# Optimization experiments

Measured on AMD Instinct MI355X. Metric: run time of the kernel, lower is better.

The kernel has to match this reference:

```python
import jax, jax.numpy as jnp
import numpy as np

DEGREE = 5
A = 1.0
B = 1.0
IN_F = 1024
OUT_F = 1024
BATCH = 8192


def setup_inputs() -> dict:
    key = jax.random.key(0)
    k1, k2, k3, k4 = jax.random.split(key, 4)
    x = jax.random.normal(k1, (BATCH, IN_F), dtype=jnp.float32)
    # base_weight ~ kaiming-uniform-ish scale
    bound_w = 1.0 / np.sqrt(IN_F)
    base_weight = jax.random.uniform(k2, (OUT_F, IN_F), dtype=jnp.float32,
                                     minval=-bound_w, maxval=bound_w)
    std = 1.0 / (IN_F * np.sqrt(DEGREE + 1))
    jacobi_coeffs = std * jax.random.normal(k3, (OUT_F, IN_F, DEGREE + 1), dtype=jnp.float32)
    bias = jax.random.uniform(k4, (OUT_F,), dtype=jnp.float32, minval=-bound_w, maxval=bound_w)
    return {"x": x, "base_weight": base_weight, "jacobi_coeffs": jacobi_coeffs, "bias": bias}


def _jacobi_polynomials(x):
    # x: (batch, in_features) -> (batch, in_features, DEGREE+1)
    t = jnp.tanh(x)
    polys = [jnp.ones_like(t)]
    if DEGREE >= 1:
        polys.append(0.5 * (2.0 * (A + 1.0) * t + (A - B)))
    for k in range(2, DEGREE + 1):
        # recurrence coefficients (matching torch loop where k = written index)
        alpha_n = 2.0 * k * (k + A + B) * (2 * k + A + B - 2)
        beta_n = (2 * k + A + B - 1) * (A ** 2 - B ** 2)
        gamma_n = (2 * k + A + B - 2) * (2 * k + A + B - 1) * (2 * k + A + B)
        delta_n = 2.0 * (k + A - 1) * (k + B - 1) * (2 * k + A + B)
        Acoef = (beta_n + alpha_n * t) / gamma_n
        Bcoef = delta_n / gamma_n
        polys.append(Acoef * polys[k - 1] - Bcoef * polys[k - 2])
    return jnp.stack(polys, axis=-1)


def reference(x, base_weight, jacobi_coeffs, bias):
    # base branch: SiLU then linear
    base_out = jax.nn.silu(x) @ base_weight.T  # (b, out)
    # jacobi branch
    P = _jacobi_polynomials(x)  # (b, in, deg+1)
    jac_out = jnp.einsum('bik,oik->bo', P, jacobi_coeffs)
    return base_out + jac_out + bias
```

## Files before the change

kernel.cpp:

```cpp
#include <hip/hip_runtime.h>
#include <hip/hip_bf16.h>
#include <cstdint>
#include <cstddef>

#define BATCH   8192
#define IN_F    1024
#define OUT_F   1024
#define KAUG    (6 * 1024)

typedef __bf16 bf16x8 __attribute__((ext_vector_type(8)));
typedef float  f32x4  __attribute__((ext_vector_type(4)));

static constexpr size_t WAUG_B    = (size_t)OUT_F * KAUG * 2;
static constexpr size_t BIAS2_OFF = WAUG_B;
static constexpr size_t AAUG_OFF  = WAUG_B + 4096;
static constexpr size_t AAUG_B    = (size_t)BATCH * KAUG * 2;
static constexpr size_t MMAP_OFF  = AAUG_OFF + AAUG_B;
static constexpr size_t NMAP_OFF  = MMAP_OFF + 1024;

__device__ __constant__ float JAC_A[4] = {64.f/120.f, 180.f/336.f, 384.f/720.f, 700.f/1320.f};
__device__ __constant__ float JAC_B[4] = {48.f/120.f, 144.f/336.f, 320.f/720.f, 600.f/1320.f};

__device__ __forceinline__ unsigned short f2bf(float f)
{
    __hip_bfloat16 h = __float2bfloat16(f);
    return *(unsigned short*)&h;
}
__device__ __forceinline__ unsigned pack2(float lo, float hi)
{
    return (unsigned)f2bf(lo) | ((unsigned)f2bf(hi) << 16);
}
__device__ __forceinline__ float fast_tanh(float x)
{
    const float xc = fminf(fmaxf(x, -15.f), 15.f);
    const float e  = __expf(2.f * xc);
    return (e - 1.f) / (e + 1.f);
}

__global__ void probe_layout(int* __restrict__ mmap, int* __restrict__ nmap)
{
    __shared__ __align__(16) __hip_bfloat16 A1[16 * 32], B1[16 * 32];
    __shared__ __align__(16) __hip_bfloat16 A2[16 * 32], B2[16 * 32];
    const int lane = threadIdx.x;
    for (int e = lane; e < 512; e += 64) {
        const int m = e >> 5, k = e & 31;
        A1[e] = __float2bfloat16((k == 0) ? (float)(m + 1) : 0.f);
        B1[e] = __float2bfloat16((k == 0) ? 1.f : 0.f);
        A2[e] = __float2bfloat16((k == 0) ? 1.f : 0.f);
        B2[e] = __float2bfloat16((k == 0) ? (float)(m + 1) : 0.f);
    }
    __syncthreads();
    const int quad = lane >> 4, mr = lane & 15;
    const int fi = mr * 4 + quad;
    f32x4 z = {};
    f32x4 d1 = __builtin_amdgcn_mfma_f32_16x16x32_bf16(((const bf16x8*)A1)[fi], ((const bf16x8*)B1)[fi], z, 0, 0, 0);
    f32x4 d2 = __builtin_amdgcn_mfma_f32_16x16x32_bf16(((const bf16x8*)A2)[fi], ((const bf16x8*)B2)[fi], z, 0, 0, 0);
#pragma unroll
    for (int r = 0; r < 4; ++r) {
        mmap[lane * 4 + r] = (int)(d1[r] + 0.5f) - 1;
        nmap[lane * 4 + r] = (int)(d2[r] + 0.5f) - 1;
    }
}

__global__ void prep_all(const float* __restrict__ X,
                         const float* __restrict__ W,
                         const float* __restrict__ C,
                         const float* __restrict__ bias,
                         __hip_bfloat16* __restrict__ Aaug,
                         __hip_bfloat16* __restrict__ Waug,
                         float* __restrict__ bias2)
{
    const int bid = blockIdx.x;
    const int tid = threadIdx.x;
    if (bid < OUT_F) {
        const int o = bid;
        const int i = tid * 4;
        const size_t wbase = (size_t)o * KAUG;

        const float4 wv = *(const float4*)(W + (size_t)o * IN_F + i);
        ((uint2*)&Waug[wbase + i])[0] = make_uint2(pack2(wv.x, wv.y), pack2(wv.z, wv.w));

        float f[24];
        const float2* cp = (const float2*)(C + ((size_t)o * IN_F + i) * 6);
#pragma unroll
        for (int q = 0; q < 12; ++q) { const float2 v = cp[q]; f[q * 2] = v.x; f[q * 2 + 1] = v.y; }
#pragma unroll
        for (int j = 1; j <= 5; ++j) {
            ((uint2*)&Waug[wbase + (size_t)j * IN_F + i])[0] =
                make_uint2(pack2(f[0 + j], f[6 + j]), pack2(f[12 + j], f[18 + j]));
        }
        float s = f[0] + f[6] + f[12] + f[18];
#pragma unroll
        for (int off = 32; off > 0; off >>= 1) s += __shfl_down(s, off, 64);
        __shared__ float red[4];
        if ((tid & 63) == 0) red[tid >> 6] = s;
        __syncthreads();
        if (tid == 0) bias2[o] = bias[o] + red[0] + red[1] + red[2] + red[3];
    } else {
        const int gid = (bid - OUT_F) * 256 + tid;
        const int b   = gid >> 7;
        const int i8  = (gid & 127) * 8;
        const float4 x0 = *(const float4*)(X + (size_t)b * IN_F + i8);
        const float4 x1 = *(const float4*)(X + (size_t)b * IN_F + i8 + 4);
        const float sx[8] = {x0.x, x0.y, x0.z, x0.w, x1.x, x1.y, x1.z, x1.w};
        const size_t base = (size_t)b * KAUG + i8;

        float sil[8], t[8], pm1[8], pm2[8];
#pragma unroll
        for (int e = 0; e < 8; ++e) {
            sil[e] = sx[e] / (1.f + __expf(-sx[e]));
            t[e]   = fast_tanh(sx[e]);
            pm2[e] = 1.f; pm1[e] = 2.f * t[e];
        }
        *(uint4*)&Aaug[base] = make_uint4(pack2(sil[0], sil[1]), pack2(sil[2], sil[3]),
                                          pack2(sil[4], sil[5]), pack2(sil[6], sil[7]));
        *(uint4*)&Aaug[base + IN_F] = make_uint4(pack2(pm1[0], pm1[1]), pack2(pm1[2], pm1[3]),
                                                 pack2(pm1[4], pm1[5]), pack2(pm1[6], pm1[7]));
#pragma unroll
        for (int k = 2; k <= 5; ++k) {
#pragma unroll
            for (int e = 0; e < 8; ++e) {
                const float pk = JAC_A[k - 2] * t[e] * pm1[e] - JAC_B[k - 2] * pm2[e];
                pm2[e] = pm1[e]; pm1[e] = pk;
            }
            *(uint4*)&Aaug[base + (size_t)k * IN_F] =
                make_uint4(pack2(pm1[0], pm1[1]), pack2(pm1[2], pm1[3]),
                           pack2(pm1[4], pm1[5]), pack2(pm1[6], pm1[7]));
        }
    }
}

__device__ __forceinline__ void async_load16(const void* g, void* l)
{
    __builtin_amdgcn_global_load_lds(
        (const __attribute__((address_space(1))) void*)g,
        (__attribute__((address_space(3))) void*)l,
        16, 0, 0);
}

__global__ __launch_bounds__(256, 2)
void gemm_kan(const __hip_bfloat16* __restrict__ Aaug,
              const __hip_bfloat16* __restrict__ Waug,
              const float* __restrict__ bias2,
              const int* __restrict__ mmap,
              const int* __restrict__ nmap,
              float* __restrict__ out)
{
    __shared__ __align__(16) __hip_bfloat16 As[2][128 * 32], As2[2][128 * 32];
    __shared__ __align__(16) __hip_bfloat16 Bs[2][128 * 32], Bs2[2][128 * 32];

    const int tid  = threadIdx.x;
    const int lane = tid & 63;
    const int wave = tid >> 6;
    const int wm = wave & 1, wn = wave >> 1;
    const int mBase = blockIdx.x * 128;
    const int nBase = blockIdx.y * 128;

    const int srow = tid >> 2;
    const int chnk = tid & 3;
    const int scol = (chnk ^ ((srow >> 1) & 3)) * 8;
    const __hip_bfloat16* gA0 = Aaug + (size_t)(mBase + srow) * KAUG + scol;
    const __hip_bfloat16* gA1 = gA0 + (size_t)64 * KAUG;
    const __hip_bfloat16* gB0 = Waug + (size_t)(nBase + srow) * KAUG + scol;
    const __hip_bfloat16* gB1 = gB0 + (size_t)64 * KAUG;
    const int woff = wave * 1024;

    f32x4 acc[4][4] = {};
    const int quad = lane >> 4, mr = lane & 15;
    const int qsw  = quad ^ ((mr >> 1) & 3);

    {
        async_load16(gA0, (char*)As[0] + woff);
        async_load16(gA1, (char*)As[0] + woff + 4096);
        async_load16(gB0, (char*)Bs[0] + woff);
        async_load16(gB1, (char*)Bs[0] + woff + 4096);
        async_load16(gA0 + 32, (char*)As2[0] + woff);
        async_load16(gA1 + 32, (char*)As2[0] + woff + 4096);
        async_load16(gB0 + 32, (char*)Bs2[0] + woff);
        async_load16(gB1 + 32, (char*)Bs2[0] + woff + 4096);
    }
    __syncthreads();

    for (int k0 = 0; k0 < KAUG; k0 += 64) {
        const int cur = (k0 >> 6) & 1;
        const int nxt = cur ^ 1;
        if (k0 + 64 < KAUG) {
            const int kn = k0 + 64;
            async_load16(gA0 + kn, (char*)As[nxt] + woff);
            async_load16(gA1 + kn, (char*)As[nxt] + woff + 4096);
            async_load16(gB0 + kn, (char*)Bs[nxt] + woff);
            async_load16(gB1 + kn, (char*)Bs[nxt] + woff + 4096);
            async_load16(gA0 + kn + 32, (char*)As2[nxt] + woff);
            async_load16(gA1 + kn + 32, (char*)As2[nxt] + woff + 4096);
            async_load16(gB0 + kn + 32, (char*)Bs2[nxt] + woff);
            async_load16(gB1 + kn + 32, (char*)Bs2[nxt] + woff + 4096);
        }
        {
            const bf16x8* AsV = (const bf16x8*)As[cur];
            const bf16x8* BsV = (const bf16x8*)Bs[cur];
            bf16x8 a[4], b[4];
#pragma unroll
            for (int t = 0; t < 4; ++t) a[t] = AsV[(wm * 64 + t * 16 + mr) * 4 + qsw];
#pragma unroll
            for (int t = 0; t < 4; ++t) b[t] = BsV[(wn * 64 + t * 16 + mr) * 4 + qsw];
#pragma unroll
            for (int i = 0; i < 4; ++i)
#pragma unroll
                for (int jj = 0; jj < 4; ++jj)
                    acc[i][jj] = __builtin_amdgcn_mfma_f32_16x16x32_bf16(a[i], b[jj], acc[i][jj], 0, 0, 0);
        }
        {
            const bf16x8* AsV = (const bf16x8*)As2[cur];
            const bf16x8* BsV = (const bf16x8*)Bs2[cur];
            bf16x8 a[4], b[4];
#pragma unroll
            for (int t = 0; t < 4; ++t) a[t] = AsV[(wm * 64 + t * 16 + mr) * 4 + qsw];
#pragma unroll
            for (int t = 0; t < 4; ++t) b[t] = BsV[(wn * 64 + t * 16 + mr) * 4 + qsw];
#pragma unroll
            for (int i = 0; i < 4; ++i)
#pragma unroll
                for (int jj = 0; jj < 4; ++jj)
                    acc[i][jj] = __builtin_amdgcn_mfma_f32_16x16x32_bf16(a[i], b[jj], acc[i][jj], 0, 0, 0);
        }
        __syncthreads();
    }

    const int4 mv = ((const int4*)mmap)[lane];
    const int4 nv = ((const int4*)nmap)[lane];
    const int mm[4] = {mv.x, mv.y, mv.z, mv.w};
    const int nn[4] = {nv.x, nv.y, nv.z, nv.w};
#pragma unroll
    for (int i = 0; i < 4; ++i) {
#pragma unroll
        for (int jj = 0; jj < 4; ++jj) {
#pragma unroll
            for (int r = 0; r < 4; ++r) {
                const int row = mBase + wm * 64 + i * 16 + mm[r];
                const int col = nBase + wn * 64 + jj * 16 + nn[r];
                out[(size_t)row * OUT_F + col] = acc[i][jj][r] + bias2[col];
            }
        }
    }
}


extern "C" void kernel_launch(void* const* d_in, const int* in_sizes, int n_in,
                              void* d_out, int out_size, void* d_ws, size_t ws_size,
                              hipStream_t stream)
{
    (void)out_size; (void)ws_size;
    const float* x    = (const float*)d_in[0];
    const float* W    = (const float*)d_in[1];
    const float* C    = (const float*)d_in[2];
    const float* bias = (const float*)d_in[3];
    for (int i = 0; i < n_in; ++i) {
        if      (in_sizes[i] == BATCH * IN_F)     x    = (const float*)d_in[i];
        else if (in_sizes[i] == OUT_F * IN_F)     W    = (const float*)d_in[i];
        else if (in_sizes[i] == OUT_F * IN_F * 6) C    = (const float*)d_in[i];
        else if (in_sizes[i] == OUT_F)            bias = (const float*)d_in[i];
    }
    float* out = (float*)d_out;
    char* ws = (char*)d_ws;
    __hip_bfloat16* Waug  = (__hip_bfloat16*)ws;
    float*          bias2 = (float*)(ws + BIAS2_OFF);
    __hip_bfloat16* Aaug  = (__hip_bfloat16*)(ws + AAUG_OFF);
    int*            mmap  = (int*)(ws + MMAP_OFF);
    int*            nmap  = (int*)(ws + NMAP_OFF);

    probe_layout<<<dim3(1), dim3(64), 0, stream>>>(mmap, nmap);
    prep_all<<<dim3(OUT_F + (BATCH * IN_F) / 2048), dim3(256), 0, stream>>>(
        x, W, C, bias, Aaug, Waug, bias2);
    gemm_kan<<<dim3(BATCH / 128, OUT_F / 128), dim3(256), 0, stream>>>(
        Aaug, Waug, bias2, mmap, nmap, out);
}
```

Baseline: 227.6 us.

## Restructure GEMM to 256x128 tiles with triple-buffered LDS and phased MFMA

The GEMM moves from a 128x128 tile with 4 waves and double buffering to a 256x128 tile with 8 waves and a three-stage LDS ring in dynamic shared memory. Each K-tile of 64 is split into four phases that interleave async global-to-LDS loads with MFMA work, using raw s_barrier, explicit waitcnt and s_setprio to keep the matrix units busy. The XOR swizzle is widened to 8 chunks per row. This aims to raise reuse of each loaded tile and hide memory latency, at the cost of 144KB LDS per block (one block per CU), more barriers, and hand-managed vmcnt counting that could be fragile.

```diff
diff --git a/kernel.cpp b/kernel.cpp
--- a/kernel.cpp
+++ b/kernel.cpp
@@ -138,7 +138,11 @@
         16, 0, 0);
 }
 
-__global__ __launch_bounds__(256, 2)
+#define ABYTES 32768
+#define TILEB  49152
+#define NT     96
+
+__global__ __launch_bounds__(512, 2)
 void gemm_kan(const __hip_bfloat16* __restrict__ Aaug,
               const __hip_bfloat16* __restrict__ Waug,
               const float* __restrict__ bias2,
@@ -146,85 +150,121 @@
               const int* __restrict__ nmap,
               float* __restrict__ out)
 {
-    __shared__ __align__(16) __hip_bfloat16 As[2][128 * 32], As2[2][128 * 32];
-    __shared__ __align__(16) __hip_bfloat16 Bs[2][128 * 32], Bs2[2][128 * 32];
+    extern __shared__ __align__(16) char smem[];
 
     const int tid  = threadIdx.x;
     const int lane = tid & 63;
     const int wave = tid >> 6;
-    const int wm = wave & 1, wn = wave >> 1;
-    const int mBase = blockIdx.x * 128;
+    const int wm = wave >> 1, wn = wave & 1;
+    const int mBase = blockIdx.x * 256;
     const int nBase = blockIdx.y * 128;
 
-    const int srow = tid >> 2;
-    const int chnk = tid & 3;
-    const int scol = (chnk ^ ((srow >> 1) & 3)) * 8;
-    const __hip_bfloat16* gA0 = Aaug + (size_t)(mBase + srow) * KAUG + scol;
-    const __hip_bfloat16* gA1 = gA0 + (size_t)64 * KAUG;
-    const __hip_bfloat16* gB0 = Waug + (size_t)(nBase + srow) * KAUG + scol;
-    const __hip_bfloat16* gB1 = gB0 + (size_t)64 * KAUG;
-    const int woff = wave * 1024;
+    const __hip_bfloat16* gA[4]; int lA[4];
+#pragma unroll
+    for (int j = 0; j < 4; ++j) {
+        const int idx = (j * 8 + wave) * 64 + lane;
+        const int row = idx >> 3, sc = idx & 7, gc = sc ^ (row & 7);
+        gA[j] = Aaug + (size_t)(mBase + row) * KAUG + gc * 8;
+        lA[j] = (j * 8 + wave) * 1024;
+    }
+    const __hip_bfloat16* gB[2]; int lB[2];
+#pragma unroll
+    for (int j = 0; j < 2; ++j) {
+        const int idx = (j * 8 + wave) * 64 + lane;
+        const int row = idx >> 3, sc = idx & 7, gc = sc ^ (row & 7);
+        gB[j] = Waug + (size_t)(nBase + row) * KAUG + gc * 8;
+        lB[j] = ABYTES + (j * 8 + wave) * 1024;
+    }
+
+    const int quad = lane >> 4, mr = lane & 15;
+    int rA[4], rB[4], csw[2];
+#pragma unroll
+    for (int t = 0; t < 4; ++t) rA[t] = (wm * 64 + t * 16 + mr) * 128;
+#pragma unroll
+    for (int t = 0; t < 4; ++t) rB[t] = ABYTES + (wn * 64 + t * 16 + mr) * 128;
+    csw[0] = ((0 + quad) ^ (mr & 7)) * 16;
+    csw[1] = ((4 + quad) ^ (mr & 7)) * 16;
 
     f32x4 acc[4][4] = {};
-    const int quad = lane >> 4, mr = lane & 15;
-    const int qsw  = quad ^ ((mr >> 1) & 3);
-
+
+#pragma unroll
+    for (int j = 0; j < 4; ++j) async_load16(gA[j], smem + lA[j]);
+#pragma unroll
+    for (int j = 0; j < 2; ++j) async_load16(gB[j], smem + lB[j]);
+#pragma unroll
+    for (int j = 0; j < 4; ++j) async_load16(gA[j] + 64, smem + TILEB + lA[j]);
+#pragma unroll
+    for (int j = 0; j < 2; ++j) async_load16(gB[j] + 64, smem + TILEB + lB[j]);
+    asm volatile("s_waitcnt vmcnt(6)" ::: "memory");
+    __builtin_amdgcn_s_barrier();
+
+#define KTILE(CB, SB, KK, DOST)                                              \
+    {                                                                        \
+        _Pragma("unroll")                                                    \
+        for (int ph = 0; ph < 4; ++ph) {                                     \
+            const int mh = ph >> 1, nh = ph & 1;                             \
+            bf16x8 fa[2][2], fb[2][2];                                       \
+            _Pragma("unroll")                                                \
+            for (int tf = 0; tf < 2; ++tf) {                                 \
+                _Pragma("unroll")                                            \
+                for (int ks = 0; ks < 2; ++ks) {                             \
+                    fa[tf][ks] = *(const bf16x8*)((CB) + rA[mh * 2 + tf] + csw[ks]); \
+                    fb[tf][ks] = *(const bf16x8*)((CB) + rB[nh * 2 + tf] + csw[ks]); \
+                }                                                            \
+            }                                                                \
+            if (DOST) {                                                      \
+                if (ph == 0) { async_load16(gA[0] + (KK), (SB) + lA[0]);     \
+                               async_load16(gA[1] + (KK), (SB) + lA[1]); }   \
+                if (ph == 1) { async_load16(gA[2] + (KK), (SB) + lA[2]);     \
+                               async_load16(gA[3] + (KK), (SB) + lA[3]); }   \
+                if (ph == 2) { async_load16(gB[0] + (KK), (SB) + lB[0]); }   \
+                if (ph == 3) { async_load16(gB[1] + (KK), (SB) + lB[1]); }   \
+            }                                                                \
+            __builtin_amdgcn_s_barrier();                                    \
+            asm volatile("s_waitcnt lgkmcnt(0)" ::: "memory");               \
+            __builtin_amdgcn_s_setprio(1);                                   \
+            _Pragma("unroll")                                                \
+            for (int tm = 0; tm < 2; ++tm) {                                 \
+                _Pragma("unroll")                                            \
+                for (int tn = 0; tn < 2; ++tn) {                             \
+                    _Pragma("unroll")                                        \
+                    for (int ks = 0; ks < 2; ++ks)                           \
+                        acc[mh * 2 + tm][nh * 2 + tn] =                      \
+                            __builtin_amdgcn_mfma_f32_16x16x32_bf16(         \
+                                fa[tm][ks], fb[tn][ks],                      \
+                                acc[mh * 2 + tm][nh * 2 + tn], 0, 0, 0);     \
+                }                                                            \
+            }                                                                \
+            __builtin_amdgcn_s_setprio(0);                                   \
+            if (ph < 3) __builtin_amdgcn_s_barrier();                        \
+        }                                                                    \
+    }
+
+    int buf = 0, nb = 2;
+    size_t kk = 128;
+#pragma unroll 1
+    for (int t = 0; t < NT - 2; ++t) {
+        const char* Cb = smem + buf * TILEB;
+        char*       Sb = smem + nb  * TILEB;
+        KTILE(Cb, Sb, kk, 1);
+        asm volatile("s_waitcnt vmcnt(6)" ::: "memory");
+        __builtin_amdgcn_s_barrier();
+        buf = (buf == 2) ? 0 : buf + 1;
+        nb  = (nb  == 2) ? 0 : nb  + 1;
+        kk += 64;
+    }
     {
-        async_load16(gA0, (char*)As[0] + woff);
-        async_load16(gA1, (char*)As[0] + woff + 4096);
-        async_load16(gB0, (char*)Bs[0] + woff);
-        async_load16(gB1, (char*)Bs[0] + woff + 4096);
-        async_load16(gA0 + 32, (char*)As2[0] + woff);
-        async_load16(gA1 + 32, (char*)As2[0] + woff + 4096);
-        async_load16(gB0 + 32, (char*)Bs2[0] + woff);
-        async_load16(gB1 + 32, (char*)Bs2[0] + woff + 4096);
-    }
-    __syncthreads();
-
-    for (int k0 = 0; k0 < KAUG; k0 += 64) {
-        const int cur = (k0 >> 6) & 1;
-        const int nxt = cur ^ 1;
-        if (k0 + 64 < KAUG) {
-            const int kn = k0 + 64;
-            async_load16(gA0 + kn, (char*)As[nxt] + woff);
-            async_load16(gA1 + kn, (char*)As[nxt] + woff + 4096);
-            async_load16(gB0 + kn, (char*)Bs[nxt] + woff);
-            async_load16(gB1 + kn, (char*)Bs[nxt] + woff + 4096);
-            async_load16(gA0 + kn + 32, (char*)As2[nxt] + woff);
-            async_load16(gA1 + kn + 32, (char*)As2[nxt] + woff + 4096);
-            async_load16(gB0 + kn + 32, (char*)Bs2[nxt] + woff);
-            async_load16(gB1 + kn + 32, (char*)Bs2[nxt] + woff + 4096);
-        }
-        {
-            const bf16x8* AsV = (const bf16x8*)As[cur];
-            const bf16x8* BsV = (const bf16x8*)Bs[cur];
-            bf16x8 a[4], b[4];
-#pragma unroll
-            for (int t = 0; t < 4; ++t) a[t] = AsV[(wm * 64 + t * 16 + mr) * 4 + qsw];
-#pragma unroll
-            for (int t = 0; t < 4; ++t) b[t] = BsV[(wn * 64 + t * 16 + mr) * 4 + qsw];
-#pragma unroll
-            for (int i = 0; i < 4; ++i)
-#pragma unroll
-                for (int jj = 0; jj < 4; ++jj)
-                    acc[i][jj] = __builtin_amdgcn_mfma_f32_16x16x32_bf16(a[i], b[jj], acc[i][jj], 0, 0, 0);
-        }
-        {
-            const bf16x8* AsV = (const bf16x8*)As2[cur];
-            const bf16x8* BsV = (const bf16x8*)Bs2[cur];
-            bf16x8 a[4], b[4];
-#pragma unroll
-            for (int t = 0; t < 4; ++t) a[t] = AsV[(wm * 64 + t * 16 + mr) * 4 + qsw];
-#pragma unroll
-            for (int t = 0; t < 4; ++t) b[t] = BsV[(wn * 64 + t * 16 + mr) * 4 + qsw];
-#pragma unroll
-            for (int i = 0; i < 4; ++i)
-#pragma unroll
-                for (int jj = 0; jj < 4; ++jj)
-                    acc[i][jj] = __builtin_amdgcn_mfma_f32_16x16x32_bf16(a[i], b[jj], acc[i][jj], 0, 0, 0);
-        }
-        __syncthreads();
-    }
+        const char* Cb = smem + buf * TILEB;
+        KTILE(Cb, (char*)nullptr, 0, 0);
+        asm volatile("s_waitcnt vmcnt(0)" ::: "memory");
+        __builtin_amdgcn_s_barrier();
+        buf = (buf == 2) ? 0 : buf + 1;
+    }
+    {
+        const char* Cb = smem + buf * TILEB;
+        KTILE(Cb, (char*)nullptr, 0, 0);
+    }
+#undef KTILE
 
     const int4 mv = ((const int4*)mmap)[lane];
     const int4 nv = ((const int4*)nmap)[lane];
@@ -268,9 +308,17 @@
     int*            mmap  = (int*)(ws + MMAP_OFF);
     int*            nmap  = (int*)(ws + NMAP_OFF);
 
+    static bool smem_attr_done = false;
+    if (!smem_attr_done) {
+        (void)hipFuncSetAttribute((const void*)gemm_kan,
+                                  hipFuncAttributeMaxDynamicSharedMemorySize,
+                                  3 * TILEB);
+        smem_attr_done = true;
+    }
+
     probe_layout<<<dim3(1), dim3(64), 0, stream>>>(mmap, nmap);
     prep_all<<<dim3(OUT_F + (BATCH * IN_F) / 2048), dim3(256), 0, stream>>>(
         x, W, C, bias, Aaug, Waug, bias2);
-    gemm_kan<<<dim3(BATCH / 128, OUT_F / 128), dim3(256), 0, stream>>>(
+    gemm_kan<<<dim3(BATCH / 256, OUT_F / 128), dim3(512), 3 * TILEB, stream>>>(
         Aaug, Waug, bias2, mmap, nmap, out);
 }
```

Result: no change. 231.1 us (+1.5%).

## Fuse Jacobi/SiLU feature expansion into GEMM A-tile load, interleave K layout

Applied to the files above, without the earlier changes.

The separate pass that wrote the expanded bf16 activation matrix (8192x6144) to global memory is removed. Each GEMM block now reads raw fp32 x, computes SiLU, tanh and the Jacobi polynomials on the fly, and writes interleaved bf16 features into shared memory. Weights are repacked so each input feature's six coefficients sit next to each other, matching the interleaved A layout. This drops a large global write and re-read, but every N-block (eight per M-row) recomputes the transcendentals, and the A tile is now single-buffered with two barriers per step, which may reduce overlap.

```diff
diff --git a/kernel.cpp b/kernel.cpp
--- a/kernel.cpp
+++ b/kernel.cpp
@@ -7,15 +7,14 @@
 #define IN_F    1024
 #define OUT_F   1024
 #define KAUG    (6 * 1024)
+#define NSTEP   64
 
 typedef __bf16 bf16x8 __attribute__((ext_vector_type(8)));
 typedef float  f32x4  __attribute__((ext_vector_type(4)));
 
 static constexpr size_t WAUG_B    = (size_t)OUT_F * KAUG * 2;
 static constexpr size_t BIAS2_OFF = WAUG_B;
-static constexpr size_t AAUG_OFF  = WAUG_B + 4096;
-static constexpr size_t AAUG_B    = (size_t)BATCH * KAUG * 2;
-static constexpr size_t MMAP_OFF  = AAUG_OFF + AAUG_B;
+static constexpr size_t MMAP_OFF  = WAUG_B + 4096;
 static constexpr size_t NMAP_OFF  = MMAP_OFF + 1024;
 
 __device__ __constant__ float JAC_A[4] = {64.f/120.f, 180.f/336.f, 384.f/720.f, 700.f/1320.f};
@@ -62,72 +61,43 @@
     }
 }
 
-__global__ void prep_all(const float* __restrict__ X,
-                         const float* __restrict__ W,
-                         const float* __restrict__ C,
-                         const float* __restrict__ bias,
-                         __hip_bfloat16* __restrict__ Aaug,
-                         __hip_bfloat16* __restrict__ Waug,
-                         float* __restrict__ bias2)
-{
-    const int bid = blockIdx.x;
+__global__ void prep_w(const float* __restrict__ W,
+                       const float* __restrict__ C,
+                       const float* __restrict__ bias,
+                       __hip_bfloat16* __restrict__ Waug,
+                       float* __restrict__ bias2)
+{
+    const int o = blockIdx.x;
     const int tid = threadIdx.x;
-    if (bid < OUT_F) {
-        const int o = bid;
-        const int i = tid * 4;
-        const size_t wbase = (size_t)o * KAUG;
-
-        const float4 wv = *(const float4*)(W + (size_t)o * IN_F + i);
-        ((uint2*)&Waug[wbase + i])[0] = make_uint2(pack2(wv.x, wv.y), pack2(wv.z, wv.w));
-
-        float f[24];
-        const float2* cp = (const float2*)(C + ((size_t)o * IN_F + i) * 6);
-#pragma unroll
-        for (int q = 0; q < 12; ++q) { const float2 v = cp[q]; f[q * 2] = v.x; f[q * 2 + 1] = v.y; }
-#pragma unroll
-        for (int j = 1; j <= 5; ++j) {
-            ((uint2*)&Waug[wbase + (size_t)j * IN_F + i])[0] =
-                make_uint2(pack2(f[0 + j], f[6 + j]), pack2(f[12 + j], f[18 + j]));
-        }
-        float s = f[0] + f[6] + f[12] + f[18];
-#pragma unroll
-        for (int off = 32; off > 0; off >>= 1) s += __shfl_down(s, off, 64);
-        __shared__ float red[4];
-        if ((tid & 63) == 0) red[tid >> 6] = s;
-        __syncthreads();
-        if (tid == 0) bias2[o] = bias[o] + red[0] + red[1] + red[2] + red[3];
-    } else {
-        const int gid = (bid - OUT_F) * 256 + tid;
-        const int b   = gid >> 7;
-        const int i8  = (gid & 127) * 8;
-        const float4 x0 = *(const float4*)(X + (size_t)b * IN_F + i8);
-        const float4 x1 = *(const float4*)(X + (size_t)b * IN_F + i8 + 4);
-        const float sx[8] = {x0.x, x0.y, x0.z, x0.w, x1.x, x1.y, x1.z, x1.w};
-        const size_t base = (size_t)b * KAUG + i8;
-
-        float sil[8], t[8], pm1[8], pm2[8];
-#pragma unroll
-        for (int e = 0; e < 8; ++e) {
-            sil[e] = sx[e] / (1.f + __expf(-sx[e]));
-            t[e]   = fast_tanh(sx[e]);
-            pm2[e] = 1.f; pm1[e] = 2.f * t[e];
-        }
-        *(uint4*)&Aaug[base] = make_uint4(pack2(sil[0], sil[1]), pack2(sil[2], sil[3]),
-                                          pack2(sil[4], sil[5]), pack2(sil[6], sil[7]));
-        *(uint4*)&Aaug[base + IN_F] = make_uint4(pack2(pm1[0], pm1[1]), pack2(pm1[2], pm1[3]),
-                                                 pack2(pm1[4], pm1[5]), pack2(pm1[6], pm1[7]));
-#pragma unroll
-        for (int k = 2; k <= 5; ++k) {
-#pragma unroll
-            for (int e = 0; e < 8; ++e) {
-                const float pk = JAC_A[k - 2] * t[e] * pm1[e] - JAC_B[k - 2] * pm2[e];
-                pm2[e] = pm1[e]; pm1[e] = pk;
-            }
-            *(uint4*)&Aaug[base + (size_t)k * IN_F] =
-                make_uint4(pack2(pm1[0], pm1[1]), pack2(pm1[2], pm1[3]),
-                           pack2(pm1[4], pm1[5]), pack2(pm1[6], pm1[7]));
-        }
-    }
+    const int i = tid * 4;
+
+    const float4 wv = *(const float4*)(W + (size_t)o * IN_F + i);
+    const float w4[4] = {wv.x, wv.y, wv.z, wv.w};
+
+    float f[24];
+    const float2* cp = (const float2*)(C + ((size_t)o * IN_F + i) * 6);
+#pragma unroll
+    for (int q = 0; q < 12; ++q) { const float2 v = cp[q]; f[q * 2] = v.x; f[q * 2 + 1] = v.y; }
+
+    unsigned pk[12];
+#pragma unroll
+    for (int q = 0; q < 4; ++q) {
+        pk[q * 3 + 0] = pack2(w4[q],        f[q * 6 + 1]);
+        pk[q * 3 + 1] = pack2(f[q * 6 + 2], f[q * 6 + 3]);
+        pk[q * 3 + 2] = pack2(f[q * 6 + 4], f[q * 6 + 5]);
+    }
+    uint4* dst = (uint4*)(Waug + (size_t)o * KAUG + (size_t)tid * 24);
+    dst[0] = make_uint4(pk[0], pk[1], pk[2],  pk[3]);
+    dst[1] = make_uint4(pk[4], pk[5], pk[6],  pk[7]);
+    dst[2] = make_uint4(pk[8], pk[9], pk[10], pk[11]);
+
+    float s = f[0] + f[6] + f[12] + f[18];
+#pragma unroll
+    for (int off = 32; off > 0; off >>= 1) s += __shfl_down(s, off, 64);
+    __shared__ float red[4];
+    if ((tid & 63) == 0) red[tid >> 6] = s;
+    __syncthreads();
+    if (tid == 0) bias2[o] = bias[o] + red[0] + red[1] + red[2] + red[3];
 }
 
 __device__ __forceinline__ void async_load16(const void* g, void* l)
@@ -138,16 +108,19 @@
         16, 0, 0);
 }
 
+#define AS_B    24576
+#define BS_B    24576
+#define SMEM_B  (AS_B + 2 * BS_B)
+
 __global__ __launch_bounds__(256, 2)
-void gemm_kan(const __hip_bfloat16* __restrict__ Aaug,
+void gemm_kan(const float* __restrict__ X,
               const __hip_bfloat16* __restrict__ Waug,
               const float* __restrict__ bias2,
               const int* __restrict__ mmap,
               const int* __restrict__ nmap,
               float* __restrict__ out)
 {
-    __shared__ __align__(16) __hip_bfloat16 As[2][128 * 32], As2[2][128 * 32];
-    __shared__ __align__(16) __hip_bfloat16 Bs[2][128 * 32], Bs2[2][128 * 32];
+    extern __shared__ __align__(16) char smem[];
 
     const int tid  = threadIdx.x;
     const int lane = tid & 63;
@@ -156,74 +129,77 @@
     const int mBase = blockIdx.x * 128;
     const int nBase = blockIdx.y * 128;
 
-    const int srow = tid >> 2;
-    const int chnk = tid & 3;
-    const int scol = (chnk ^ ((srow >> 1) & 3)) * 8;
-    const __hip_bfloat16* gA0 = Aaug + (size_t)(mBase + srow) * KAUG + scol;
-    const __hip_bfloat16* gA1 = gA0 + (size_t)64 * KAUG;
-    const __hip_bfloat16* gB0 = Waug + (size_t)(nBase + srow) * KAUG + scol;
-    const __hip_bfloat16* gB1 = gB0 + (size_t)64 * KAUG;
-    const int woff = wave * 1024;
+    const float* gx = X + (size_t)(mBase + (tid >> 1)) * IN_F + (tid & 1) * 8;
+    char* const aw = smem + (tid >> 1) * 192 + (tid & 1) * 96;
+
+    const __hip_bfloat16* gB[6]; int lB[6];
+#pragma unroll
+    for (int q = 0; q < 6; ++q) {
+        const int ci = (q * 4 + wave) * 64 + lane;
+        const int br = ci / 12, bc = ci - br * 12;
+        gB[q] = Waug + (size_t)(nBase + br) * KAUG + bc * 8;
+        lB[q] = AS_B + (q * 4 + wave) * 1024;
+    }
+
+    const int quad = lane >> 4, mr = lane & 15;
+    const int aoff = (wm * 64 + mr) * 12 + quad;
+    const int boff = (AS_B / 16) + (wn * 64 + mr) * 12 + quad;
 
     f32x4 acc[4][4] = {};
-    const int quad = lane >> 4, mr = lane & 15;
-    const int qsw  = quad ^ ((mr >> 1) & 3);
-
-    {
-        async_load16(gA0, (char*)As[0] + woff);
-        async_load16(gA1, (char*)As[0] + woff + 4096);
-        async_load16(gB0, (char*)Bs[0] + woff);
-        async_load16(gB1, (char*)Bs[0] + woff + 4096);
-        async_load16(gA0 + 32, (char*)As2[0] + woff);
-        async_load16(gA1 + 32, (char*)As2[0] + woff + 4096);
-        async_load16(gB0 + 32, (char*)Bs2[0] + woff);
-        async_load16(gB1 + 32, (char*)Bs2[0] + woff + 4096);
-    }
-    __syncthreads();
-
-    for (int k0 = 0; k0 < KAUG; k0 += 64) {
-        const int cur = (k0 >> 6) & 1;
-        const int nxt = cur ^ 1;
-        if (k0 + 64 < KAUG) {
-            const int kn = k0 + 64;
-            async_load16(gA0 + kn, (char*)As[nxt] + woff);
-            async_load16(gA1 + kn, (char*)As[nxt] + woff + 4096);
-            async_load16(gB0 + kn, (char*)Bs[nxt] + woff);
-            async_load16(gB1 + kn, (char*)Bs[nxt] + woff + 4096);
-            async_load16(gA0 + kn + 32, (char*)As2[nxt] + woff);
-            async_load16(gA1 + kn + 32, (char*)As2[nxt] + woff + 4096);
-            async_load16(gB0 + kn + 32, (char*)Bs2[nxt] + woff);
-            async_load16(gB1 + kn + 32, (char*)Bs2[nxt] + woff + 4096);
-        }
-        {
-            const bf16x8* AsV = (const bf16x8*)As[cur];
-            const bf16x8* BsV = (const bf16x8*)Bs[cur];
+
+    float4 xc0 = *(const float4*)(gx);
+    float4 xc1 = *(const float4*)(gx + 4);
+#pragma unroll
+    for (int q = 0; q < 6; ++q) async_load16(gB[q], smem + lB[q]);
+
+#pragma unroll 1
+    for (int t = 0; t < NSTEP; ++t) {
+        const float xs[8] = {xc0.x, xc0.y, xc0.z, xc0.w, xc1.x, xc1.y, xc1.z, xc1.w};
+        unsigned pk[24];
+#pragma unroll
+        for (int e = 0; e < 8; ++e) {
+            const float x  = xs[e];
+            const float s  = x / (1.f + __expf(-x));
+            const float tt = fast_tanh(x);
+            const float p1 = 2.f * tt;
+            const float p2 = JAC_A[0] * tt * p1 - JAC_B[0];
+            const float p3 = JAC_A[1] * tt * p2 - JAC_B[1] * p1;
+            const float p4 = JAC_A[2] * tt * p3 - JAC_B[2] * p2;
+            const float p5 = JAC_A[3] * tt * p4 - JAC_B[3] * p3;
+            pk[e * 3 + 0] = pack2(s,  p1);
+            pk[e * 3 + 1] = pack2(p2, p3);
+            pk[e * 3 + 2] = pack2(p4, p5);
+        }
+        __syncthreads();
+#pragma unroll
+        for (int j = 0; j < 6; ++j)
+            *(uint4*)(aw + j * 16) = make_uint4(pk[j * 4], pk[j * 4 + 1],
+                                                pk[j * 4 + 2], pk[j * 4 + 3]);
+        __syncthreads();
+
+        if (t + 1 < NSTEP) {
+            char* const bs = smem + ((t + 1) & 1) * BS_B;
+#pragma unroll
+            for (int q = 0; q < 6; ++q) async_load16(gB[q] + (t + 1) * 96, bs + lB[q]);
+            xc0 = *(const float4*)(gx + (t + 1) * 16);
+            xc1 = *(const float4*)(gx + (t + 1) * 16 + 4);
+        }
+
+        const bf16x8* V = (const bf16x8*)smem;
+        const int bo = boff + (t & 1) * (BS_B / 16);
+#pragma unroll
+        for (int kc = 0; kc < 3; ++kc) {
             bf16x8 a[4], b[4];
 #pragma unroll
-            for (int t = 0; t < 4; ++t) a[t] = AsV[(wm * 64 + t * 16 + mr) * 4 + qsw];
-#pragma unroll
-            for (int t = 0; t < 4; ++t) b[t] = BsV[(wn * 64 + t * 16 + mr) * 4 + qsw];
+            for (int t4 = 0; t4 < 4; ++t4) a[t4] = V[aoff + t4 * 192 + kc * 4];
+#pragma unroll
+            for (int t4 = 0; t4 < 4; ++t4) b[t4] = V[bo + t4 * 192 + kc * 4];
 #pragma unroll
             for (int i = 0; i < 4; ++i)
 #pragma unroll
                 for (int jj = 0; jj < 4; ++jj)
                     acc[i][jj] = __builtin_amdgcn_mfma_f32_16x16x32_bf16(a[i], b[jj], acc[i][jj], 0, 0, 0);
         }
-        {
-            const bf16x8* AsV = (const bf16x8*)As2[cur];
-            const bf16x8* BsV = (const bf16x8*)Bs2[cur];
-            bf16x8 a[4], b[4];
-#pragma unroll
-            for (int t = 0; t < 4; ++t) a[t] = AsV[(wm * 64 + t * 16 + mr) * 4 + qsw];
-#pragma unroll
-            for (int t = 0; t < 4; ++t) b[t] = BsV[(wn * 64 + t * 16 + mr) * 4 + qsw];
-#pragma unroll
-            for (int i = 0; i < 4; ++i)
-#pragma unroll
-                for (int jj = 0; jj < 4; ++jj)
-                    acc[i][jj] = __builtin_amdgcn_mfma_f32_16x16x32_bf16(a[i], b[jj], acc[i][jj], 0, 0, 0);
-        }
-        __syncthreads();
     }
 
     const int4 mv = ((const int4*)mmap)[lane];
@@ -264,13 +240,19 @@
     char* ws = (char*)d_ws;
     __hip_bfloat16* Waug  = (__hip_bfloat16*)ws;
     float*          bias2 = (float*)(ws + BIAS2_OFF);
-    __hip_bfloat16* Aaug  = (__hip_bfloat16*)(ws + AAUG_OFF);
     int*            mmap  = (int*)(ws + MMAP_OFF);
     int*            nmap  = (int*)(ws + NMAP_OFF);
 
+    static bool smem_attr_done = false;
+    if (!smem_attr_done) {
+        (void)hipFuncSetAttribute((const void*)gemm_kan,
+                                  hipFuncAttributeMaxDynamicSharedMemorySize,
+                                  SMEM_B);
+        smem_attr_done = true;
+    }
+
     probe_layout<<<dim3(1), dim3(64), 0, stream>>>(mmap, nmap);
-    prep_all<<<dim3(OUT_F + (BATCH * IN_F) / 2048), dim3(256), 0, stream>>>(
-        x, W, C, bias, Aaug, Waug, bias2);
-    gemm_kan<<<dim3(BATCH / 128, OUT_F / 128), dim3(256), 0, stream>>>(
-        Aaug, Waug, bias2, mmap, nmap, out);
-}
+    prep_w<<<dim3(OUT_F), dim3(256), 0, stream>>>(W, C, bias, Waug, bias2);
+    gemm_kan<<<dim3(BATCH / 128, OUT_F / 128), dim3(256), SMEM_B, stream>>>(
+        x, Waug, bias2, mmap, nmap, out);
+}
```

Result: slower. 281.5 us (+23.7%).
